# Performance work log

Hardware: AMD Instinct MI355X
Metric: run time of the kernel (lower is better)

Reference implementation:

```python
import jax, jax.numpy as jnp
import numpy as np

D_MODEL = 1024
N_HEADS = 16
THETA = 10000.0


def _rope(x, pos):
    # x: [b, h, s, d], d even. Interleaved pairs: x1 = even dims, x2 = odd dims.
    d = x.shape[-1]
    half = d // 2
    inv_freq = THETA ** (-(jnp.arange(half, dtype=jnp.float32) / half))
    ang = pos[:, None].astype(jnp.float32) * inv_freq[None, :]  # [s, half]
    cos, sin = jnp.cos(ang), jnp.sin(ang)
    x1 = x[..., 0::2]
    x2 = x[..., 1::2]
    r1 = x1 * cos - x2 * sin
    r2 = x1 * sin + x2 * cos
    return jnp.stack((r1, r2), axis=-1).reshape(x.shape)


def setup_inputs() -> dict:
    key = jax.random.key(0)
    ks = jax.random.split(key, 5)
    b, s, d = 2, 2048, D_MODEL
    sigma = np.sqrt(2.0 / (d + d))
    return {
        "x": jax.random.normal(ks[0], (b, s, d), dtype=jnp.float32),
        "Wq": jax.random.normal(ks[1], (d, d), dtype=jnp.float32) * sigma,
        "Wk": jax.random.normal(ks[2], (d, d), dtype=jnp.float32) * sigma,
        "Wv": jax.random.normal(ks[3], (d, d), dtype=jnp.float32) * sigma,
        "Wo": jax.random.normal(ks[4], (d, d), dtype=jnp.float32) * sigma,
    }


def reference(x, Wq, Wk, Wv, Wo):
    b, s, d = x.shape
    h = N_HEADS
    dh = d // h

    def proj(W):
        y = jnp.einsum('bsn,mn->bsm', x, W)  # Linear: x @ W.T
        return y.reshape(b, s, h, dh).transpose(0, 2, 1, 3)  # [b,h,s,dh]

    Q, K, V = proj(Wq), proj(Wk), proj(Wv)
    pos = jnp.arange(s)
    Q = _rope(Q, pos)
    K = _rope(K, pos)

    scores = jnp.einsum('bhnd,bhmd->bhnm', Q, K) / jnp.sqrt(jnp.float32(dh))
    causal = jnp.tril(jnp.ones((s, s), dtype=bool))
    scores = jnp.where(causal, scores, -jnp.inf)
    attn = jax.nn.softmax(scores, axis=-1)
    out = jnp.einsum('bhnm,bhmd->bhnd', attn, V)
    out = out.transpose(0, 2, 1, 3).reshape(b, s, d)
    return jnp.einsum('bsn,mn->bsm', out, Wo)
```

## Files before the change

### kernel.cpp

```cpp
#include <hip/hip_runtime.h>
#include <hip/hip_bf16.h>
#include <math.h>

#define B_    2
#define S_    2048
#define D_    1024
#define H_    16
#define DH_   64
#define HALF_ 32
#define M_    (B_ * S_)

typedef __attribute__((ext_vector_type(8))) short bf16x8;
typedef __attribute__((ext_vector_type(4))) float f32x4;

#define MFMA(a, b, c) __builtin_amdgcn_mfma_f32_16x16x32_bf16((a), (b), (c), 0, 0, 0)

#if defined(__has_builtin)
#if __has_builtin(__builtin_amdgcn_global_load_lds)
#define HAVE_GLOAD_LDS 1
#endif
#endif

#ifdef HAVE_GLOAD_LDS
#define GLOAD16(gp, lp)                                                        \
  __builtin_amdgcn_global_load_lds(                                            \
      (const __attribute__((address_space(1))) void*)(gp),                     \
      (__attribute__((address_space(3))) void*)(lp), 16, 0, 0)
#endif

__device__ __forceinline__ ushort f2bf(float f) {
  uint u = __float_as_uint(f);
  u += 0x7fffu + ((u >> 16) & 1u);
  return (ushort)(u >> 16);
}
__device__ __forceinline__ float bf2f(ushort h) {
  return __uint_as_float(((uint)h) << 16);
}
__device__ __forceinline__ void split4(float4 v, uint2* hi, uint2* lo) {
  ushort h0 = f2bf(v.x), h1 = f2bf(v.y), h2 = f2bf(v.z), h3 = f2bf(v.w);
  hi->x = (uint)h0 | ((uint)h1 << 16);
  hi->y = (uint)h2 | ((uint)h3 << 16);
  ushort e0 = f2bf(v.x - bf2f(h0)), e1 = f2bf(v.y - bf2f(h1));
  ushort e2 = f2bf(v.z - bf2f(h2)), e3 = f2bf(v.w - bf2f(h3));
  lo->x = (uint)e0 | ((uint)e1 << 16);
  lo->y = (uint)e2 | ((uint)e3 << 16);
}

__global__ void split_x_kernel(const float4* __restrict__ src,
                               uint2* __restrict__ hi, uint2* __restrict__ lo,
                               int n4) {
  int i = blockIdx.x * blockDim.x + threadIdx.x;
  if (i >= n4) return;
  uint2 h, l;
  split4(src[i], &h, &l);
  hi[i] = h;
  lo[i] = l;
}

__global__ void split_w_kernel(const float4* __restrict__ w0,
                               const float4* __restrict__ w1,
                               const float4* __restrict__ w2,
                               const float4* __restrict__ w3,
                               uint2* __restrict__ h0, uint2* __restrict__ l0,
                               uint2* __restrict__ h1, uint2* __restrict__ l1,
                               uint2* __restrict__ h2, uint2* __restrict__ l2,
                               uint2* __restrict__ h3, uint2* __restrict__ l3,
                               int n4) {
  int i = blockIdx.x * blockDim.x + threadIdx.x;
  if (i >= n4) return;
  int y = blockIdx.y;
  const float4* src = (y == 0) ? w0 : (y == 1) ? w1 : (y == 2) ? w2 : w3;
  uint2* hi = (y == 0) ? h0 : (y == 1) ? h1 : (y == 2) ? h2 : h3;
  uint2* lo = (y == 0) ? l0 : (y == 1) ? l1 : (y == 2) ? l2 : l3;
  uint2 h, l;
  split4(src[i], &h, &l);
  hi[i] = h;
  lo[i] = l;
}

__global__ void rope_tab_kernel(float2* __restrict__ tab) {
  int idx = blockIdx.x * blockDim.x + threadIdx.x;
  if (idx >= S_ * HALF_) return;
  int s = idx >> 5;
  int f = idx & (HALF_ - 1);
  float invf = powf(10000.0f, -((float)f) / (float)HALF_);
  float ang = (float)s * invf;
  tab[idx] = make_float2(cosf(ang), sinf(ang));
}

#ifdef HAVE_GLOAD_LDS
#define STAGE_TILES(Asrc_h, Asrc_l, Bsrc_h, Bsrc_l, rowA0, rowB0, kt)          \
  do {                                                                         \
    _Pragma("unroll") for (int p = 0; p < 2; ++p) {                            \
      int cch = wv * 2 + p;                      \
      int lrow = cch * 16 + (l >> 2);               \
      int sl = (l & 3) ^ (lrow & 3);                \
      size_t ga = (size_t)((rowA0) + lrow) * D_ + (kt) + sl * 8;               \
      size_t gb = (size_t)((rowB0) + lrow) * D_ + (kt) + sl * 8;               \
      GLOAD16((Asrc_h) + ga, (char*)Ah + cch * 1024);                          \
      GLOAD16((Asrc_l) + ga, (char*)Al + cch * 1024);                          \
      GLOAD16((Bsrc_h) + gb, (char*)Bh + cch * 1024);                          \
      GLOAD16((Bsrc_l) + gb, (char*)Bl + cch * 1024);                          \
    }                                                                          \
  } while (0)
#else
#define STAGE_TILES(Asrc_h, Asrc_l, Bsrc_h, Bsrc_l, rowA0, rowB0, kt)          \
  do {                                                                         \
    _Pragma("unroll") for (int p = 0; p < 2; ++p) {                            \
      int idx = t + p * 256;                                                   \
      int row = idx >> 2;                                                      \
      int ch = idx & 3;                                                        \
      int off = (row << 5) + ((ch ^ (row & 3)) << 3);                          \
      size_t ga = (size_t)((rowA0) + row) * D_ + (kt) + ch * 8;                \
      size_t gb = (size_t)((rowB0) + row) * D_ + (kt) + ch * 8;                \
      *(uint4*)&Ah[off] = *(const uint4*)&(Asrc_h)[ga];                        \
      *(uint4*)&Al[off] = *(const uint4*)&(Asrc_l)[ga];                        \
      *(uint4*)&Bh[off] = *(const uint4*)&(Bsrc_h)[gb];                        \
      *(uint4*)&Bl[off] = *(const uint4*)&(Bsrc_l)[gb];                        \
    }                                                                          \
  } while (0)
#endif

__global__ __launch_bounds__(256) void qkv_mfma_kernel(
    const ushort* __restrict__ xh, const ushort* __restrict__ xl,
    const ushort* __restrict__ Wqh, const ushort* __restrict__ Wql,
    const ushort* __restrict__ Wkh, const ushort* __restrict__ Wkl,
    const ushort* __restrict__ Wvh, const ushort* __restrict__ Wvl,
    ushort* __restrict__ Qh, ushort* __restrict__ Ql,
    ushort* __restrict__ Kh, ushort* __restrict__ Kl,
    ushort* __restrict__ Vth, ushort* __restrict__ Vtl,
    const float2* __restrict__ tab) {
  __shared__ __align__(16) ushort Ah[128 * 32], Al[128 * 32];
  __shared__ __align__(16) ushort Bh[128 * 32], Bl[128 * 32];

  const int which = blockIdx.z;
  const ushort* __restrict__ Wh = (which == 0) ? Wqh : (which == 1) ? Wkh : Wvh;
  const ushort* __restrict__ Wl = (which == 0) ? Wql : (which == 1) ? Wkl : Wvl;

  const int lin = (int)blockIdx.y * 8 + (int)blockIdx.x;
  const int wid = (lin & 7) * 32 + (lin >> 3);
  const int r0 = (wid >> 3) * 128;
  const int c0 = (wid & 7) * 128;

  const int t = threadIdx.x;
  const int l = t & 63, wv = t >> 6;
  const int g = l >> 4, li = l & 15;
  const int wr = (wv >> 1) * 64, wc = (wv & 1) * 64;

  f32x4 zero4 = {0.f, 0.f, 0.f, 0.f};
  f32x4 acc[4][4];
#pragma unroll
  for (int i = 0; i < 4; ++i)
#pragma unroll
    for (int j = 0; j < 4; ++j) acc[i][j] = zero4;

  for (int kt = 0; kt < D_; kt += 32) {
    __syncthreads();
    STAGE_TILES(xh, xl, Wh, Wl, r0, c0, kt);
    __syncthreads();

    bf16x8 ah[4], al[4], bh[4], bl[4];
#pragma unroll
    for (int fm = 0; fm < 4; ++fm) {
      int row = wr + fm * 16 + li;
      int idx = (row << 5) + ((g ^ (row & 3)) << 3);
      ah[fm] = *(const bf16x8*)&Ah[idx];
      al[fm] = *(const bf16x8*)&Al[idx];
    }
#pragma unroll
    for (int fn = 0; fn < 4; ++fn) {
      int row = wc + fn * 16 + li;
      int idx = (row << 5) + ((g ^ (row & 3)) << 3);
      bh[fn] = *(const bf16x8*)&Bh[idx];
      bl[fn] = *(const bf16x8*)&Bl[idx];
    }
    __builtin_amdgcn_s_setprio(1);
#pragma unroll
    for (int fm = 0; fm < 4; ++fm)
#pragma unroll
      for (int fn = 0; fn < 4; ++fn) {
        acc[fm][fn] = MFMA(ah[fm], bh[fn], acc[fm][fn]);
        acc[fm][fn] = MFMA(ah[fm], bl[fn], acc[fm][fn]);
        acc[fm][fn] = MFMA(al[fm], bh[fn], acc[fm][fn]);
      }
    __builtin_amdgcn_s_setprio(0);
  }

  if (which < 2) {
#pragma unroll
    for (int fm = 0; fm < 4; ++fm) {
#pragma unroll
      for (int reg = 0; reg < 4; ++reg) {
        int r = r0 + wr + fm * 16 + g * 4 + reg;
        int b = r >> 11, s = r & (S_ - 1);
#pragma unroll
        for (int fn = 0; fn < 4; ++fn) {
          float v = acc[fm][fn][reg];
          int c = c0 + wc + fn * 16 + li;
          int h = c >> 6, dc = c & 63;
          float pr = __shfl_xor(v, 1);
          int f = dc >> 1;
          float2 cssn = tab[(s << 5) + f];
          float res = (c & 1) ? (pr * cssn.y + v * cssn.x)
                              : (v * cssn.x - pr * cssn.y);
          size_t o = ((size_t)((b << 4) + h) * S_ + s) * DH_ + dc;
          ushort hi = f2bf(res);
          ushort lo = f2bf(res - bf2f(hi));
          if (which == 0) { Qh[o] = hi; Ql[o] = lo; }
          else            { Kh[o] = hi; Kl[o] = lo; }
        }
      }
    }
  } else {
#pragma unroll
    for (int fm = 0; fm < 4; ++fm) {
      int rbase = r0 + wr + fm * 16 + g * 4;
      int b = rbase >> 11, s0 = rbase & (S_ - 1);
#pragma unroll
      for (int fn = 0; fn < 4; ++fn) {
        int c = c0 + wc + fn * 16 + li;
        int h = c >> 6, dc = c & 63;
        ushort hv[4], lv[4];
#pragma unroll
        for (int reg = 0; reg < 4; ++reg) {
          float v = acc[fm][fn][reg];
          hv[reg] = f2bf(v);
          lv[reg] = f2bf(v - bf2f(hv[reg]));
        }
        size_t o = ((size_t)((b << 4) + h) * DH_ + dc) * S_ + s0;
        *(ushort4*)&Vth[o] = make_ushort4(hv[0], hv[1], hv[2], hv[3]);
        *(ushort4*)&Vtl[o] = make_ushort4(lv[0], lv[1], lv[2], lv[3]);
      }
    }
  }
}

__global__ __launch_bounds__(256) void attn_mfma_kernel(
    const ushort* __restrict__ Qh, const ushort* __restrict__ Ql,
    const ushort* __restrict__ Kh, const ushort* __restrict__ Kl,
    const ushort* __restrict__ Vth, const ushort* __restrict__ Vtl,
    ushort* __restrict__ aoh, ushort* __restrict__ aol) {
  __shared__ __align__(16) ushort Ps[4][2][32 * 64];

  const int lin = (int)blockIdx.y * 16 + (int)blockIdx.x;
  const int wid = (lin & 7) * 64 + (lin >> 3);
  const int bh = wid >> 4;
  const int qi = 15 - (wid & 15);

  const int t = threadIdx.x, w = t >> 6, l = t & 63;
  const int g = l >> 4, li = l & 15;
  const int R0 = qi * 128 + w * 32;

  const size_t qkBase = (size_t)bh * S_ * DH_;
  const size_t vBase  = (size_t)bh * DH_ * S_;

  bf16x8 qh[2][2], ql[2][2];
#pragma unroll
  for (int fm = 0; fm < 2; ++fm)
#pragma unroll
    for (int kc = 0; kc < 2; ++kc) {
      size_t off = qkBase + (size_t)(R0 + fm * 16 + li) * DH_ + kc * 32 + g * 8;
      qh[fm][kc] = *(const bf16x8*)&Qh[off];
      ql[fm][kc] = *(const bf16x8*)&Ql[off];
    }

  f32x4 zero4 = {0.f, 0.f, 0.f, 0.f};
  float m[2][4], ls[2][4];
  f32x4 o[2][4];
#pragma unroll
  for (int fm = 0; fm < 2; ++fm) {
#pragma unroll
    for (int r = 0; r < 4; ++r) { m[fm][r] = -INFINITY; ls[fm][r] = 0.f; }
#pragma unroll
    for (int fd = 0; fd < 4; ++fd) o[fm][fd] = zero4;
  }

  const int nT = 2 * qi + 1 + (w >> 1);

  for (int t2 = 0; t2 < nT; ++t2) {
    const int kv0 = t2 * 64;
    const bool diag = (t2 == nT - 1);

    f32x4 sc[2][4];
#pragma unroll
    for (int fm = 0; fm < 2; ++fm)
#pragma unroll
      for (int fn = 0; fn < 4; ++fn) sc[fm][fn] = zero4;

#pragma unroll
    for (int fn = 0; fn < 4; ++fn) {
#pragma unroll
      for (int kc = 0; kc < 2; ++kc) {
        size_t off =
            qkBase + (size_t)(kv0 + fn * 16 + li) * DH_ + kc * 32 + g * 8;
        bf16x8 kh = *(const bf16x8*)&Kh[off];
        bf16x8 kl = *(const bf16x8*)&Kl[off];
        __builtin_amdgcn_s_setprio(1);
#pragma unroll
        for (int fm = 0; fm < 2; ++fm) {
          sc[fm][fn] = MFMA(qh[fm][kc], kh, sc[fm][fn]);
          sc[fm][fn] = MFMA(qh[fm][kc], kl, sc[fm][fn]);
          sc[fm][fn] = MFMA(ql[fm][kc], kh, sc[fm][fn]);
        }
        __builtin_amdgcn_s_setprio(0);
      }
    }

#pragma unroll
    for (int fm = 0; fm < 2; ++fm)
#pragma unroll
      for (int fn = 0; fn < 4; ++fn)
#pragma unroll
        for (int r = 0; r < 4; ++r) {
          float s = sc[fm][fn][r] * 0.125f;
          if (diag) {
            int colg = kv0 + fn * 16 + li;
            int rowg = R0 + fm * 16 + g * 4 + r;
            if (colg > rowg) s = -1e30f;
          }
          sc[fm][fn][r] = s;
        }

#pragma unroll
    for (int fm = 0; fm < 2; ++fm) {
#pragma unroll
      for (int r = 0; r < 4; ++r) {
        float ml = fmaxf(fmaxf(sc[fm][0][r], sc[fm][1][r]),
                         fmaxf(sc[fm][2][r], sc[fm][3][r]));
        ml = fmaxf(ml, __shfl_xor(ml, 1));
        ml = fmaxf(ml, __shfl_xor(ml, 2));
        ml = fmaxf(ml, __shfl_xor(ml, 4));
        ml = fmaxf(ml, __shfl_xor(ml, 8));
        float mn = fmaxf(m[fm][r], ml);
        float al = __expf(m[fm][r] - mn);
        m[fm][r] = mn;
        float p[4];
        float rs = 0.f;
#pragma unroll
        for (int fn = 0; fn < 4; ++fn) {
          p[fn] = __expf(sc[fm][fn][r] - mn);
          rs += p[fn];
        }
        rs += __shfl_xor(rs, 1);
        rs += __shfl_xor(rs, 2);
        rs += __shfl_xor(rs, 4);
        rs += __shfl_xor(rs, 8);
        ls[fm][r] = ls[fm][r] * al + rs;
#pragma unroll
        for (int fd = 0; fd < 4; ++fd) o[fm][fd][r] *= al;

        int prow = fm * 16 + g * 4 + r;
#pragma unroll
        for (int fn = 0; fn < 4; ++fn) {
          int idx = ((prow << 6) + fn * 16 + li) ^ ((prow & 7) << 3);
          ushort hi = f2bf(p[fn]);
          Ps[w][0][idx] = hi;
          Ps[w][1][idx] = f2bf(p[fn] - bf2f(hi));
        }
      }
    }
    __builtin_amdgcn_wave_barrier();

#pragma unroll
    for (int kc = 0; kc < 2; ++kc) {
      bf16x8 pah[2], pal[2];
#pragma unroll
      for (int fm = 0; fm < 2; ++fm) {
        int ridx = fm * 16 + li;
        int idx = (ridx << 6) + ((kc * 32 + g * 8) ^ ((ridx & 7) << 3));
        pah[fm] = *(const bf16x8*)&Ps[w][0][idx];
        pal[fm] = *(const bf16x8*)&Ps[w][1][idx];
      }
#pragma unroll
      for (int fd = 0; fd < 4; ++fd) {
        size_t off =
            vBase + (size_t)(fd * 16 + li) * S_ + kv0 + kc * 32 + g * 8;
        bf16x8 vh = *(const bf16x8*)&Vth[off];
        bf16x8 vl = *(const bf16x8*)&Vtl[off];
        __builtin_amdgcn_s_setprio(1);
#pragma unroll
        for (int fm = 0; fm < 2; ++fm) {
          o[fm][fd] = MFMA(pah[fm], vh, o[fm][fd]);
          o[fm][fd] = MFMA(pah[fm], vl, o[fm][fd]);
          o[fm][fd] = MFMA(pal[fm], vh, o[fm][fd]);
        }
        __builtin_amdgcn_s_setprio(0);
      }
    }
    __builtin_amdgcn_wave_barrier();
  }

  const int b = bh >> 4, h = bh & 15;
#pragma unroll
  for (int fm = 0; fm < 2; ++fm)
#pragma unroll
    for (int fd = 0; fd < 4; ++fd)
#pragma unroll
      for (int r = 0; r < 4; ++r) {
        int srow = R0 + fm * 16 + g * 4 + r;
        int c = h * DH_ + fd * 16 + li;
        float v = o[fm][fd][r] / ls[fm][r];
        size_t oo = ((size_t)b * S_ + srow) * D_ + c;
        ushort hi = f2bf(v);
        aoh[oo] = hi;
        aol[oo] = f2bf(v - bf2f(hi));
      }
}

__global__ __launch_bounds__(256) void out_mfma_kernel(
    const ushort* __restrict__ Aph, const ushort* __restrict__ Apl,
    const ushort* __restrict__ Wh, const ushort* __restrict__ Wl,
    float* __restrict__ out) {
  __shared__ __align__(16) ushort Ah[128 * 32], Al[128 * 32];
  __shared__ __align__(16) ushort Bh[128 * 32], Bl[128 * 32];

  const int lin = (int)blockIdx.y * 8 + (int)blockIdx.x;
  const int wid = (lin & 7) * 32 + (lin >> 3);
  const int r0 = (wid >> 3) * 128;
  const int c0 = (wid & 7) * 128;

  const int t = threadIdx.x;
  const int l = t & 63, wv = t >> 6;
  const int g = l >> 4, li = l & 15;
  const int wr = (wv >> 1) * 64, wc = (wv & 1) * 64;

  f32x4 zero4 = {0.f, 0.f, 0.f, 0.f};
  f32x4 acc[4][4];
#pragma unroll
  for (int i = 0; i < 4; ++i)
#pragma unroll
    for (int j = 0; j < 4; ++j) acc[i][j] = zero4;

  for (int kt = 0; kt < D_; kt += 32) {
    __syncthreads();
    STAGE_TILES(Aph, Apl, Wh, Wl, r0, c0, kt);
    __syncthreads();

    bf16x8 ah[4], al[4], bh[4], bl[4];
#pragma unroll
    for (int fm = 0; fm < 4; ++fm) {
      int row = wr + fm * 16 + li;
      int idx = (row << 5) + ((g ^ (row & 3)) << 3);
      ah[fm] = *(const bf16x8*)&Ah[idx];
      al[fm] = *(const bf16x8*)&Al[idx];
    }
#pragma unroll
    for (int fn = 0; fn < 4; ++fn) {
      int row = wc + fn * 16 + li;
      int idx = (row << 5) + ((g ^ (row & 3)) << 3);
      bh[fn] = *(const bf16x8*)&Bh[idx];
      bl[fn] = *(const bf16x8*)&Bl[idx];
    }
    __builtin_amdgcn_s_setprio(1);
#pragma unroll
    for (int fm = 0; fm < 4; ++fm)
#pragma unroll
      for (int fn = 0; fn < 4; ++fn) {
        acc[fm][fn] = MFMA(ah[fm], bh[fn], acc[fm][fn]);
        acc[fm][fn] = MFMA(ah[fm], bl[fn], acc[fm][fn]);
        acc[fm][fn] = MFMA(al[fm], bh[fn], acc[fm][fn]);
      }
    __builtin_amdgcn_s_setprio(0);
  }

#pragma unroll
  for (int fm = 0; fm < 4; ++fm)
#pragma unroll
    for (int reg = 0; reg < 4; ++reg) {
      int r = r0 + wr + fm * 16 + g * 4 + reg;
#pragma unroll
      for (int fn = 0; fn < 4; ++fn) {
        int c = c0 + wc + fn * 16 + li;
        out[(size_t)r * D_ + c] = acc[fm][fn][reg];
      }
    }
}

extern "C" void kernel_launch(void* const* d_in, const int* in_sizes, int n_in,
                              void* d_out, int out_size, void* d_ws,
                              size_t ws_size, hipStream_t stream) {
  (void)in_sizes; (void)n_in; (void)out_size; (void)ws_size;
  const float* x  = (const float*)d_in[0];
  const float* Wq = (const float*)d_in[1];
  const float* Wk = (const float*)d_in[2];
  const float* Wv = (const float*)d_in[3];
  const float* Wo = (const float*)d_in[4];
  float* out = (float*)d_out;

  const size_t NP = (size_t)B_ * H_ * S_ * DH_;
  const size_t NW = (size_t)D_ * D_;
  char* w = (char*)d_ws;
  ushort* Qh  = (ushort*)w;
  ushort* Ql  = Qh + NP;
  ushort* Kh  = Ql + NP;
  ushort* Kl  = Kh + NP;
  ushort* Vth = Kl + NP;
  ushort* Vtl = Vth + NP;
  float2* tab = (float2*)(w + 6 * NP * sizeof(ushort));
  ushort* Wqh = (ushort*)(w + 6 * NP * sizeof(ushort) +
                          (size_t)S_ * HALF_ * sizeof(float2));
  ushort* Wql = Wqh + NW;
  ushort* Wkh = Wql + NW;
  ushort* Wkl = Wkh + NW;
  ushort* Wvh = Wkl + NW;
  ushort* Wvl = Wvh + NW;
  ushort* Woh = Wvl + NW;
  ushort* Wol = Woh + NW;
  ushort* xh  = Wol + NW;
  ushort* xl  = xh + (size_t)M_ * D_;
  ushort* aoh = xh;
  ushort* aol = xl;

  rope_tab_kernel<<<(S_ * HALF_ + 255) / 256, 256, 0, stream>>>(tab);

  const int n4x = M_ * D_ / 4;
  const int n4w = D_ * D_ / 4;
  split_x_kernel<<<(n4x + 255) / 256, 256, 0, stream>>>(
      (const float4*)x, (uint2*)xh, (uint2*)xl, n4x);
  split_w_kernel<<<dim3((n4w + 255) / 256, 4), 256, 0, stream>>>(
      (const float4*)Wq, (const float4*)Wk, (const float4*)Wv,
      (const float4*)Wo,
      (uint2*)Wqh, (uint2*)Wql, (uint2*)Wkh, (uint2*)Wkl,
      (uint2*)Wvh, (uint2*)Wvl, (uint2*)Woh, (uint2*)Wol, n4w);

  qkv_mfma_kernel<<<dim3(8, 32, 3), 256, 0, stream>>>(
      xh, xl, Wqh, Wql, Wkh, Wkl, Wvh, Wvl,
      Qh, Ql, Kh, Kl, Vth, Vtl, tab);

  attn_mfma_kernel<<<dim3(16, 32), 256, 0, stream>>>(
      Qh, Ql, Kh, Kl, Vth, Vtl, aoh, aol);

  out_mfma_kernel<<<dim3(8, 32), 256, 0, stream>>>(
      aoh, aol, Woh, Wol, out);
}
```

Measured before the change: 494.9 us.

## Balance causal attention work by pairing short and long query tiles per block

Each block now takes pair index pr and gives its four waves 64-row query tiles pr and 31-pr, two waves each, with the assignment rotated per block. Every block then does the same total causal work instead of blocks near the diagonal finishing early. V fragments for the whole tile are now loaded into registers before softmax so their latency overlaps that computation, and the trailing wave barrier is removed. Holding more V registers live may raise register pressure and lower occupancy.

```diff
diff --git a/kernel.cpp b/kernel.cpp
--- a/kernel.cpp
+++ b/kernel.cpp
@@ -242,26 +242,30 @@
     ushort* __restrict__ aoh, ushort* __restrict__ aol) {
   __shared__ __align__(16) ushort Ps[4][2][32 * 64];
 
-  const int lin = (int)blockIdx.y * 16 + (int)blockIdx.x;
+  const int lin = (int)blockIdx.x;
   const int wid = (lin & 7) * 64 + (lin >> 3);
   const int bh = wid >> 4;
-  const int qi = 15 - (wid & 15);
+  const int pr = wid & 15;
 
   const int t = threadIdx.x, w = t >> 6, l = t & 63;
   const int g = l >> 4, li = l & 15;
-  const int R0 = qi * 128 + w * 32;
+
+  const int wpair = (w + pr) & 3;
+  const int qt = (wpair < 2) ? pr : (31 - pr);
+  const int R0 = qt * 64 + (wpair & 1) * 32;
+  const int nT = qt + 1;
 
   const size_t qkBase = (size_t)bh * S_ * DH_;
   const size_t vBase  = (size_t)bh * DH_ * S_;
 
-  bf16x8 qh[2][2], ql[2][2];
+  bf16x8 qfh[2][2], qfl[2][2];
 #pragma unroll
   for (int fm = 0; fm < 2; ++fm)
 #pragma unroll
     for (int kc = 0; kc < 2; ++kc) {
       size_t off = qkBase + (size_t)(R0 + fm * 16 + li) * DH_ + kc * 32 + g * 8;
-      qh[fm][kc] = *(const bf16x8*)&Qh[off];
-      ql[fm][kc] = *(const bf16x8*)&Ql[off];
+      qfh[fm][kc] = *(const bf16x8*)&Qh[off];
+      qfl[fm][kc] = *(const bf16x8*)&Ql[off];
     }
 
   f32x4 zero4 = {0.f, 0.f, 0.f, 0.f};
@@ -274,8 +278,6 @@
 #pragma unroll
     for (int fd = 0; fd < 4; ++fd) o[fm][fd] = zero4;
   }
-
-  const int nT = 2 * qi + 1 + (w >> 1);
 
   for (int t2 = 0; t2 < nT; ++t2) {
     const int kv0 = t2 * 64;
@@ -298,13 +300,24 @@
         __builtin_amdgcn_s_setprio(1);
 #pragma unroll
         for (int fm = 0; fm < 2; ++fm) {
-          sc[fm][fn] = MFMA(qh[fm][kc], kh, sc[fm][fn]);
-          sc[fm][fn] = MFMA(qh[fm][kc], kl, sc[fm][fn]);
-          sc[fm][fn] = MFMA(ql[fm][kc], kh, sc[fm][fn]);
+          sc[fm][fn] = MFMA(qfh[fm][kc], kh, sc[fm][fn]);
+          sc[fm][fn] = MFMA(qfh[fm][kc], kl, sc[fm][fn]);
+          sc[fm][fn] = MFMA(qfl[fm][kc], kh, sc[fm][fn]);
         }
         __builtin_amdgcn_s_setprio(0);
       }
     }
+
+    bf16x8 vfh[2][4], vfl[2][4];
+#pragma unroll
+    for (int kc = 0; kc < 2; ++kc)
+#pragma unroll
+      for (int fd = 0; fd < 4; ++fd) {
+        size_t off =
+            vBase + (size_t)(fd * 16 + li) * S_ + kv0 + kc * 32 + g * 8;
+        vfh[kc][fd] = *(const bf16x8*)&Vth[off];
+        vfl[kc][fd] = *(const bf16x8*)&Vtl[off];
+      }
 
 #pragma unroll
     for (int fm = 0; fm < 2; ++fm)
@@ -373,21 +386,16 @@
       }
 #pragma unroll
       for (int fd = 0; fd < 4; ++fd) {
-        size_t off =
-            vBase + (size_t)(fd * 16 + li) * S_ + kv0 + kc * 32 + g * 8;
-        bf16x8 vh = *(const bf16x8*)&Vth[off];
-        bf16x8 vl = *(const bf16x8*)&Vtl[off];
         __builtin_amdgcn_s_setprio(1);
 #pragma unroll
         for (int fm = 0; fm < 2; ++fm) {
-          o[fm][fd] = MFMA(pah[fm], vh, o[fm][fd]);
-          o[fm][fd] = MFMA(pah[fm], vl, o[fm][fd]);
-          o[fm][fd] = MFMA(pal[fm], vh, o[fm][fd]);
+          o[fm][fd] = MFMA(pah[fm], vfh[kc][fd], o[fm][fd]);
+          o[fm][fd] = MFMA(pah[fm], vfl[kc][fd], o[fm][fd]);
+          o[fm][fd] = MFMA(pal[fm], vfh[kc][fd], o[fm][fd]);
         }
         __builtin_amdgcn_s_setprio(0);
       }
     }
-    __builtin_amdgcn_wave_barrier();
   }
 
   const int b = bh >> 4, h = bh & 15;
@@ -527,7 +535,7 @@
       xh, xl, Wqh, Wql, Wkh, Wkl, Wvh, Wvl,
       Qh, Ql, Kh, Kl, Vth, Vtl, tab);
 
-  attn_mfma_kernel<<<dim3(16, 32), 256, 0, stream>>>(
+  attn_mfma_kernel<<<512, 256, 0, stream>>>(
       Qh, Ql, Kh, Kl, Vth, Vtl, aoh, aol);
 
   out_mfma_kernel<<<dim3(8, 32), 256, 0, stream>>>(
```

Result: slower. 518.3 us (+4.7%).
